# Kernel tuning notes

Hardware: AMD Instinct MI355X
Metric: run time of the kernel (lower is better)

## Reference

```python
import jax, jax.numpy as jnp
import numpy as np

M_RANGE = 2
N_CLASS = 25
IM_CHANNEL = 3


def _conv(x, kernel, pad):
    # torch F.conv2d (cross-correlation), NCHW / OIHW, stride 1, symmetric padding
    return jax.lax.conv_general_dilated(
        x, kernel, window_strides=(1, 1),
        padding=[(pad, pad), (pad, pad)],
        dimension_numbers=('NCHW', 'OIHW', 'NCHW'))


def _label2mask(motion, n_class):
    # motion: [B,1,H,W] int labels -> one-hot mask [B,n_class,H,W]
    oh = jax.nn.one_hot(motion[:, 0], n_class, dtype=jnp.float32)  # [B,H,W,K]
    return jnp.transpose(oh, (0, 3, 1, 2))


def _construct_image(im, m_mask, appear, kernel, pad):
    # im: [B,C,H,W], m_mask: [B,K,H,W], appear: [B,1,H,W]
    im = im * appear
    B, C, H, W = im.shape
    K = m_mask.shape[1]
    # fuse the per-channel / per-sample torch loops into one batched conv
    x = (im[:, :, None] * m_mask[:, None]).reshape(B * C, K, H, W)
    return _conv(x, kernel, pad).reshape(B, C, H, W)


def setup_inputs() -> dict:
    key = jax.random.key(0)
    k1, k2, k3, k4, k5 = jax.random.split(key, 5)
    B, H, W = 32, 192, 192
    return {
        'im_input_f': jax.random.normal(k1, (B, 6, H, W), dtype=jnp.float32),
        'im_input_b': jax.random.normal(k2, (B, 6, H, W), dtype=jnp.float32),
        'gt_motion_f': jax.random.randint(k3, (B, 1, H, W), 0, N_CLASS, dtype=jnp.int64),
        'gt_motion_b': jax.random.randint(k4, (B, 1, H, W), 0, N_CLASS, dtype=jnp.int64),
        'm_kernel': jax.random.uniform(k5, (1, N_CLASS, 2 * M_RANGE + 1, 2 * M_RANGE + 1), dtype=jnp.float32),
    }


def reference(im_input_f, im_input_b, gt_motion_f, gt_motion_b, m_kernel):
    mask_f = _label2mask(gt_motion_f, N_CLASS)
    mask_b = _label2mask(gt_motion_b, N_CLASS)
    seg_f = _conv(mask_f, m_kernel, M_RANGE)  # [B,1,H,W]
    seg_b = _conv(mask_b, m_kernel, M_RANGE)
    appear_f = jax.nn.relu(1.0 - jax.nn.relu(seg_f - 1.0))
    appear_b = jax.nn.relu(1.0 - jax.nn.relu(seg_b - 1.0))
    pred_f = _construct_image(im_input_f[:, -IM_CHANNEL:], mask_f, appear_f, m_kernel, M_RANGE)
    pred_b = _construct_image(im_input_b[:, -IM_CHANNEL:], mask_b, appear_b, m_kernel, M_RANGE)
    seg_f = 1.0 - jax.nn.relu(1.0 - seg_f)
    seg_b = 1.0 - jax.nn.relu(1.0 - seg_b)
    attn = (seg_f + 1e-5) / (seg_f + seg_b + 2e-5)
    pred = attn * pred_f + (1.0 - attn) * pred_b
    return (pred, mask_f, 1.0 - appear_f, attn, mask_b, 1.0 - appear_b, 1.0 - attn)
```

## Files before the change

### kernel.cpp

```cpp
#include <hip/hip_runtime.h>

typedef float f32x4 __attribute__((ext_vector_type(4)));
typedef float f32x2 __attribute__((ext_vector_type(2)));

namespace {
constexpr int BATCH = 32;
constexpr int H = 192;
constexpr int W = 192;
constexpr int HW = H * W;
constexpr int NCLS = 25;
constexpr int LUTN = 26 * 25;

constexpr int OFF_PRED   = 0;
constexpr int OFF_MASKF  = BATCH * 3 * HW;
constexpr int OFF_OMAF   = OFF_MASKF + BATCH * NCLS * HW;
constexpr int OFF_ATTN   = OFF_OMAF + BATCH * HW;
constexpr int OFF_MASKB  = OFF_ATTN + BATCH * HW;
constexpr int OFF_OMAB   = OFF_MASKB + BATCH * NCLS * HW;
constexpr int OFF_OMATTN = OFF_OMAB + BATCH * HW;

constexpr int TY = 8;
constexpr int SROWS = TY + 4;
constexpr int SW = W + 8;
constexpr int GPR = W / 4;
constexpr int NTHR = GPR * TY;
constexpr int YT = H / TY;
constexpr int NBLK = BATCH * YT;
constexpr float SENT = 2.0f * NCLS;
}

__device__ __forceinline__ void nt_store4(float* p, float a, float b, float c, float d) {
    f32x4 v = {a, b, c, d};
    __builtin_nontemporal_store(v, reinterpret_cast<f32x4*>(p));
}

__device__ __forceinline__ void lab_win12(int lw[12], const int* __restrict__ row, int xb) {
    if (xb >= 4) {
        const int4 a = *reinterpret_cast<const int4*>(row + xb - 4);
        lw[0] = a.x; lw[1] = a.y; lw[2] = a.z; lw[3] = a.w;
    } else {
        lw[0] = NCLS; lw[1] = NCLS; lw[2] = NCLS; lw[3] = NCLS;
    }
    {
        const int4 c = *reinterpret_cast<const int4*>(row + xb);
        lw[4] = c.x; lw[5] = c.y; lw[6] = c.z; lw[7] = c.w;
    }
    if (xb <= W - 8) {
        const int4 e = *reinterpret_cast<const int4*>(row + xb + 4);
        lw[8] = e.x; lw[9] = e.y; lw[10] = e.z; lw[11] = e.w;
    } else {
        lw[8] = NCLS; lw[9] = NCLS; lw[10] = NCLS; lw[11] = NCLS;
    }
}

__device__ __forceinline__ void f4_win12(float w[12], const float* __restrict__ row, int xb) {
    if (xb >= 4) {
        const float4 a = *reinterpret_cast<const float4*>(row + xb - 4);
        w[0] = a.x; w[1] = a.y; w[2] = a.z; w[3] = a.w;
    } else {
        w[0] = 0.f; w[1] = 0.f; w[2] = 0.f; w[3] = 0.f;
    }
    {
        const float4 c = *reinterpret_cast<const float4*>(row + xb);
        w[4] = c.x; w[5] = c.y; w[6] = c.z; w[7] = c.w;
    }
    if (xb <= W - 8) {
        const float4 e = *reinterpret_cast<const float4*>(row + xb + 4);
        w[8] = e.x; w[9] = e.y; w[10] = e.z; w[11] = e.w;
    } else {
        w[8] = 0.f; w[9] = 0.f; w[10] = 0.f; w[11] = 0.f;
    }
}

template <bool STORES>
__device__ __forceinline__ void conv_img(
    const float (*P)[SW], const float* __restrict__ im,
    const float* __restrict__ sk, const int lab4[4],
    float* __restrict__ mbase,
    int b, int y, int x, int r_i, int g_i, float acc[3][4])
{
    for (int dy = 0; dy < 5; ++dy) {
        const int yy = y + dy - 2;
        const bool rowok = (yy >= 0 && yy < H);

        float pw[12], v0[12], v1[12], v2[12];
        if (rowok) {
            const int srow = r_i + dy;
            *reinterpret_cast<f32x4*>(&pw[0]) =
                *reinterpret_cast<const f32x4*>(&P[srow][4 * g_i]);
            *reinterpret_cast<f32x4*>(&pw[4]) =
                *reinterpret_cast<const f32x4*>(&P[srow][4 * g_i + 4]);
            *reinterpret_cast<f32x4*>(&pw[8]) =
                *reinterpret_cast<const f32x4*>(&P[srow][4 * g_i + 8]);
            const int imo = b * (6 * HW) + 3 * HW + yy * W;
            f4_win12(v0, im + imo, x);
            f4_win12(v1, im + imo + HW, x);
            f4_win12(v2, im + imo + 2 * HW, x);
        }

        if (STORES) {
#pragma unroll
            for (int kk = 0; kk < 5; ++kk) {
                const int k = dy * 5 + kk;
                nt_store4(mbase + k * HW, lab4[0] == k ? 1.f : 0.f, lab4[1] == k ? 1.f : 0.f,
                          lab4[2] == k ? 1.f : 0.f, lab4[3] == k ? 1.f : 0.f);
            }
        }

        if (rowok) {
            int lw[12];
            float aw[12];
#pragma unroll
            for (int j = 2; j < 10; ++j) {
                const int l = (int)(pw[j] * 0.5f);
                lw[j] = l;
                aw[j] = pw[j] - 2.f * (float)l;
            }
#pragma unroll
            for (int dx = 0; dx < 5; ++dx) {
                const int base = (dy * 5 + dx) * 26;
#pragma unroll
                for (int i = 0; i < 4; ++i) {
                    const int li = i + dx + 2;
                    const float w = aw[li] * sk[base + lw[li]];
                    acc[0][i] = fmaf(w, v0[li], acc[0][i]);
                    acc[1][i] = fmaf(w, v1[li], acc[1][i]);
                    acc[2][i] = fmaf(w, v2[li], acc[2][i]);
                }
            }
        }
    }
}

__global__ __launch_bounds__(NTHR) void k_fused(
    const float* __restrict__ imF, const float* __restrict__ imB,
    const int* __restrict__ labF, const int* __restrict__ labB,
    const float* __restrict__ mk, float* __restrict__ out)
{
    __shared__ float sk[LUTN];
    __shared__ float pF[SROWS][SW];
    __shared__ float pB[SROWS][SW];

    for (int i = threadIdx.x; i < LUTN; i += NTHR) {
        const int tap = i / 26;
        const int l = i - tap * 26;
        sk[i] = (l < NCLS) ? mk[l * 25 + tap] : 0.0f;
    }
    __syncthreads();

    const int blk = blockIdx.x;
    const int by = blk % YT;
    const int b  = blk / YT;
    const int y0 = by * TY;
    const int t = threadIdx.x;
    const int r_i = t / GPR;
    const int g_i = t % GPR;
    const int y = y0 + r_i;
    const int x = 4 * g_i;
    const int pix = b * HW + y * W + x;

    const int4 lfc = *reinterpret_cast<const int4*>(labF + pix);
    const int4 lbc = *reinterpret_cast<const int4*>(labB + pix);
    const int lfa[4] = {lfc.x, lfc.y, lfc.z, lfc.w};
    const int lba[4] = {lbc.x, lbc.y, lbc.z, lbc.w};
    float* __restrict__ mfb = out + OFF_MASKF + b * (NCLS * HW) + y * W + x;

    float segf[4] = {}, segb[4] = {};
#pragma unroll
    for (int dy = 0; dy < 5; ++dy) {
#pragma unroll
        for (int kk = 0; kk < 5; ++kk) {
            const int k = dy * 5 + kk;
            nt_store4(mfb + k * HW, lfa[0] == k ? 1.f : 0.f, lfa[1] == k ? 1.f : 0.f,
                      lfa[2] == k ? 1.f : 0.f, lfa[3] == k ? 1.f : 0.f);
        }
        const int yy = y + dy - 2;
        if (yy >= 0 && yy < H) {
            int lwF[12], lwB[12];
            lab_win12(lwF, labF + b * HW + yy * W, x);
            lab_win12(lwB, labB + b * HW + yy * W, x);
#pragma unroll
            for (int dx = 0; dx < 5; ++dx) {
                const int base = (dy * 5 + dx) * 26;
#pragma unroll
                for (int i = 0; i < 4; ++i) {
                    segf[i] += sk[base + lwF[i + dx + 2]];
                    segb[i] += sk[base + lwB[i + dx + 2]];
                }
            }
        }
    }

    float my_at[4];
    {
        f32x4 pf, pb;
        float af[4], ab[4];
#pragma unroll
        for (int i = 0; i < 4; ++i) {
            af[i] = fmaxf(1.f - fmaxf(segf[i] - 1.f, 0.f), 0.f);
            ab[i] = fmaxf(1.f - fmaxf(segb[i] - 1.f, 0.f), 0.f);
            pf[i] = 2.f * (float)lfa[i] + af[i];
            pb[i] = 2.f * (float)lba[i] + ab[i];
            const float scf = 1.f - fmaxf(1.f - segf[i], 0.f);
            const float scb = 1.f - fmaxf(1.f - segb[i], 0.f);
            my_at[i] = (scf + 1e-5f) / (scf + scb + 2e-5f);
        }
        *reinterpret_cast<f32x4*>(&pF[r_i + 2][4 + x]) = pf;
        *reinterpret_cast<f32x4*>(&pB[r_i + 2][4 + x]) = pb;
        nt_store4(out + OFF_OMAF + pix, 1.f - af[0], 1.f - af[1], 1.f - af[2], 1.f - af[3]);
        nt_store4(out + OFF_OMAB + pix, 1.f - ab[0], 1.f - ab[1], 1.f - ab[2], 1.f - ab[3]);
        nt_store4(out + OFF_ATTN + pix, my_at[0], my_at[1], my_at[2], my_at[3]);
        nt_store4(out + OFF_OMATTN + pix, 1.f - my_at[0], 1.f - my_at[1], 1.f - my_at[2],
                  1.f - my_at[3]);
    }

    {
        const int hrow = t / 96;
        const int row = (hrow < 2) ? hrow : hrow + TY;
        const int hg = t % 96;
        const int xabs = 2 * hg;
        const int xb = xabs & ~3;
        const int off = (hg & 1) * 2;
        const int yabs = y0 + row - 2;
        f32x2 pf2 = {SENT, SENT};
        f32x2 pb2 = {SENT, SENT};
        if (yabs >= 0 && yabs < H) {
            float sf[2] = {0.f, 0.f}, sb[2] = {0.f, 0.f};
            int lf2[2], lb2[2];
            for (int dy = 0; dy < 5; ++dy) {
                const int yy = yabs + dy - 2;
                if (yy < 0 || yy >= H) continue;
                int lwF[12], lwB[12];
                lab_win12(lwF, labF + b * HW + yy * W, xb);
                lab_win12(lwB, labB + b * HW + yy * W, xb);
                if (dy == 2) {
#pragma unroll
                    for (int i = 0; i < 2; ++i) {
                        lf2[i] = lwF[4 + off + i];
                        lb2[i] = lwB[4 + off + i];
                    }
                }
#pragma unroll
                for (int dx = 0; dx < 5; ++dx) {
                    const int base = (dy * 5 + dx) * 26;
#pragma unroll
                    for (int i = 0; i < 2; ++i) {
                        sf[i] += sk[base + lwF[2 + off + i + dx]];
                        sb[i] += sk[base + lwB[2 + off + i + dx]];
                    }
                }
            }
#pragma unroll
            for (int i = 0; i < 2; ++i) {
                const float af = fmaxf(1.f - fmaxf(sf[i] - 1.f, 0.f), 0.f);
                const float ab = fmaxf(1.f - fmaxf(sb[i] - 1.f, 0.f), 0.f);
                pf2[i] = 2.f * (float)lf2[i] + af;
                pb2[i] = 2.f * (float)lb2[i] + ab;
            }
        }
        *reinterpret_cast<f32x2*>(&pF[row][4 + xabs]) = pf2;
        *reinterpret_cast<f32x2*>(&pB[row][4 + xabs]) = pb2;
    }

    if (t < 48) {
        const int arr = t & 1, side = (t >> 1) & 1, row = t >> 2;
        f32x4 s = {SENT, SENT, SENT, SENT};
        float* dst = arr ? &pB[row][side ? W + 4 : 0] : &pF[row][side ? W + 4 : 0];
        *reinterpret_cast<f32x4*>(dst) = s;
    }

    __builtin_amdgcn_sched_barrier(0);
    asm volatile("s_waitcnt lgkmcnt(0)" ::: "memory");
    __builtin_amdgcn_s_barrier();
    __builtin_amdgcn_sched_barrier(0);
    asm volatile("" ::: "memory");

    float accF[3][4] = {};
    float accB[3][4] = {};
    conv_img<false>(pF, imF, sk, lfa, nullptr, b, y, x, r_i, g_i, accF);
    conv_img<true>(pB, imB, sk, lba, out + OFF_MASKB + b * (NCLS * HW) + y * W + x,
                   b, y, x, r_i, g_i, accB);

    float* pout = out + OFF_PRED + b * (3 * HW) + y * W + x;
#pragma unroll
    for (int c = 0; c < 3; ++c) {
        float p[4];
#pragma unroll
        for (int i = 0; i < 4; ++i)
            p[i] = my_at[i] * accF[c][i] + (1.f - my_at[i]) * accB[c][i];
        nt_store4(pout + c * HW, p[0], p[1], p[2], p[3]);
    }
}

extern "C" void kernel_launch(void* const* d_in, const int* in_sizes, int n_in,
                              void* d_out, int out_size, void* d_ws, size_t ws_size,
                              hipStream_t stream) {
    const float* imF  = (const float*)d_in[0];
    const float* imB  = (const float*)d_in[1];
    const int*   labF = (const int*)d_in[2];
    const int*   labB = (const int*)d_in[3];
    const float* mk   = (const float*)d_in[4];
    float* out = (float*)d_out;

    k_fused<<<NBLK, NTHR, 0, stream>>>(imF, imB, labF, labB, mk, out);
}
```

Measured before the change: 71.02 us.

## Stage byte-packed label tiles in shared memory and enlarge row tile

Each block now loads its label rows plus a 4-row halo once into shared memory, packing four labels per 32-bit word. The segmentation conv and the halo recomputation read those packed labels instead of issuing repeated global int4 loads per tap row. The row tile grows from 8 to 12, giving 576 threads per block and fewer blocks, and block indices are swizzled across groups of eight. This adds a shared-memory fill phase and a barrier before compute, and the larger block may lower occupancy.

```diff
diff --git a/kernel.cpp b/kernel.cpp
--- a/kernel.cpp
+++ b/kernel.cpp
@@ -19,38 +19,22 @@
 constexpr int OFF_OMAB   = OFF_MASKB + BATCH * NCLS * HW;
 constexpr int OFF_OMATTN = OFF_OMAB + BATCH * HW;
 
-constexpr int TY = 8;
+constexpr int TY = 12;
 constexpr int SROWS = TY + 4;
 constexpr int SW = W + 8;
 constexpr int GPR = W / 4;
 constexpr int NTHR = GPR * TY;
 constexpr int YT = H / TY;
 constexpr int NBLK = BATCH * YT;
+constexpr int LROWS = TY + 8;
+constexpr int LW32 = 50;
 constexpr float SENT = 2.0f * NCLS;
+constexpr unsigned SENTB = 0x19191919u;
 }
 
 __device__ __forceinline__ void nt_store4(float* p, float a, float b, float c, float d) {
     f32x4 v = {a, b, c, d};
     __builtin_nontemporal_store(v, reinterpret_cast<f32x4*>(p));
-}
-
-__device__ __forceinline__ void lab_win12(int lw[12], const int* __restrict__ row, int xb) {
-    if (xb >= 4) {
-        const int4 a = *reinterpret_cast<const int4*>(row + xb - 4);
-        lw[0] = a.x; lw[1] = a.y; lw[2] = a.z; lw[3] = a.w;
-    } else {
-        lw[0] = NCLS; lw[1] = NCLS; lw[2] = NCLS; lw[3] = NCLS;
-    }
-    {
-        const int4 c = *reinterpret_cast<const int4*>(row + xb);
-        lw[4] = c.x; lw[5] = c.y; lw[6] = c.z; lw[7] = c.w;
-    }
-    if (xb <= W - 8) {
-        const int4 e = *reinterpret_cast<const int4*>(row + xb + 4);
-        lw[8] = e.x; lw[9] = e.y; lw[10] = e.z; lw[11] = e.w;
-    } else {
-        lw[8] = NCLS; lw[9] = NCLS; lw[10] = NCLS; lw[11] = NCLS;
-    }
 }
 
 __device__ __forceinline__ void f4_win12(float w[12], const float* __restrict__ row, int xb) {
@@ -138,31 +122,51 @@
     const float* __restrict__ mk, float* __restrict__ out)
 {
     __shared__ float sk[LUTN];
+    __shared__ unsigned labs[2][LROWS][LW32];
     __shared__ float pF[SROWS][SW];
     __shared__ float pB[SROWS][SW];
 
-    for (int i = threadIdx.x; i < LUTN; i += NTHR) {
-        const int tap = i / 26;
-        const int l = i - tap * 26;
-        sk[i] = (l < NCLS) ? mk[l * 25 + tap] : 0.0f;
-    }
-    __syncthreads();
-
-    const int blk = blockIdx.x;
+    const int o = blockIdx.x;
+    const int blk = (o & 7) * (NBLK / 8) + (o >> 3);
     const int by = blk % YT;
     const int b  = blk / YT;
     const int y0 = by * TY;
     const int t = threadIdx.x;
+
+    for (int i = t; i < LUTN; i += NTHR) {
+        const int tap = i / 26;
+        const int l = i - tap * 26;
+        sk[i] = (l < NCLS) ? mk[l * 25 + tap] : 0.0f;
+    }
+    for (int u = t; u < 2 * LROWS * LW32; u += NTHR) {
+        const int img = u / (LROWS * LW32);
+        const int rem = u - img * (LROWS * LW32);
+        const int row = rem / LW32;
+        const int gw = rem - row * LW32;
+        const int yg = y0 - 4 + row;
+        unsigned v = SENTB;
+        if (yg >= 0 && yg < H && gw > 0 && gw < LW32 - 1) {
+            const int* lp = (img ? labB : labF) + b * HW + yg * W + 4 * (gw - 1);
+            const int4 l4 = *reinterpret_cast<const int4*>(lp);
+            v = (unsigned)(l4.x & 255) | ((unsigned)(l4.y & 255) << 8) |
+                ((unsigned)(l4.z & 255) << 16) | ((unsigned)(l4.w & 255) << 24);
+        }
+        labs[img][row][gw] = v;
+    }
+    __syncthreads();
+
     const int r_i = t / GPR;
     const int g_i = t % GPR;
     const int y = y0 + r_i;
     const int x = 4 * g_i;
     const int pix = b * HW + y * W + x;
 
-    const int4 lfc = *reinterpret_cast<const int4*>(labF + pix);
-    const int4 lbc = *reinterpret_cast<const int4*>(labB + pix);
-    const int lfa[4] = {lfc.x, lfc.y, lfc.z, lfc.w};
-    const int lba[4] = {lbc.x, lbc.y, lbc.z, lbc.w};
+    const unsigned cf = labs[0][r_i + 4][g_i + 1];
+    const unsigned cb = labs[1][r_i + 4][g_i + 1];
+    const int lfa[4] = {(int)(cf & 255), (int)((cf >> 8) & 255),
+                        (int)((cf >> 16) & 255), (int)((cf >> 24) & 255)};
+    const int lba[4] = {(int)(cb & 255), (int)((cb >> 8) & 255),
+                        (int)((cb >> 16) & 255), (int)((cb >> 24) & 255)};
     float* __restrict__ mfb = out + OFF_MASKF + b * (NCLS * HW) + y * W + x;
 
     float segf[4] = {}, segb[4] = {};
@@ -174,19 +178,28 @@
             nt_store4(mfb + k * HW, lfa[0] == k ? 1.f : 0.f, lfa[1] == k ? 1.f : 0.f,
                       lfa[2] == k ? 1.f : 0.f, lfa[3] == k ? 1.f : 0.f);
         }
-        const int yy = y + dy - 2;
-        if (yy >= 0 && yy < H) {
-            int lwF[12], lwB[12];
-            lab_win12(lwF, labF + b * HW + yy * W, x);
-            lab_win12(lwB, labB + b * HW + yy * W, x);
-#pragma unroll
-            for (int dx = 0; dx < 5; ++dx) {
-                const int base = (dy * 5 + dx) * 26;
-#pragma unroll
-                for (int i = 0; i < 4; ++i) {
-                    segf[i] += sk[base + lwF[i + dx + 2]];
-                    segb[i] += sk[base + lwB[i + dx + 2]];
-                }
+        const int sr = r_i + dy + 2;
+        const unsigned f0 = labs[0][sr][g_i], f1 = labs[0][sr][g_i + 1],
+                       f2 = labs[0][sr][g_i + 2];
+        const unsigned h0 = labs[1][sr][g_i], h1 = labs[1][sr][g_i + 1],
+                       h2 = labs[1][sr][g_i + 2];
+        int lwF[8], lwB[8];
+#pragma unroll
+        for (int j = 0; j < 8; ++j) {
+            const int bo = 2 + j;
+            const unsigned wf = (bo < 4) ? f0 : (bo < 8 ? f1 : f2);
+            const unsigned wb = (bo < 4) ? h0 : (bo < 8 ? h1 : h2);
+            const int sh = (bo & 3) * 8;
+            lwF[j] = (int)((wf >> sh) & 255);
+            lwB[j] = (int)((wb >> sh) & 255);
+        }
+#pragma unroll
+        for (int dx = 0; dx < 5; ++dx) {
+            const int base = (dy * 5 + dx) * 26;
+#pragma unroll
+            for (int i = 0; i < 4; ++i) {
+                segf[i] += sk[base + lwF[i + dx]];
+                segb[i] += sk[base + lwB[i + dx]];
             }
         }
     }
@@ -214,55 +227,58 @@
                   1.f - my_at[3]);
     }
 
-    {
+    if (t < 384) {
         const int hrow = t / 96;
         const int row = (hrow < 2) ? hrow : hrow + TY;
         const int hg = t % 96;
-        const int xabs = 2 * hg;
-        const int xb = xabs & ~3;
-        const int off = (hg & 1) * 2;
-        const int yabs = y0 + row - 2;
-        f32x2 pf2 = {SENT, SENT};
-        f32x2 pb2 = {SENT, SENT};
-        if (yabs >= 0 && yabs < H) {
-            float sf[2] = {0.f, 0.f}, sb[2] = {0.f, 0.f};
-            int lf2[2], lb2[2];
-            for (int dy = 0; dy < 5; ++dy) {
-                const int yy = yabs + dy - 2;
-                if (yy < 0 || yy >= H) continue;
-                int lwF[12], lwB[12];
-                lab_win12(lwF, labF + b * HW + yy * W, xb);
-                lab_win12(lwB, labB + b * HW + yy * W, xb);
-                if (dy == 2) {
-#pragma unroll
-                    for (int i = 0; i < 2; ++i) {
-                        lf2[i] = lwF[4 + off + i];
-                        lb2[i] = lwB[4 + off + i];
-                    }
-                }
-#pragma unroll
-                for (int dx = 0; dx < 5; ++dx) {
-                    const int base = (dy * 5 + dx) * 26;
-#pragma unroll
-                    for (int i = 0; i < 2; ++i) {
-                        sf[i] += sk[base + lwF[2 + off + i + dx]];
-                        sb[i] += sk[base + lwB[2 + off + i + dx]];
-                    }
-                }
-            }
-#pragma unroll
-            for (int i = 0; i < 2; ++i) {
-                const float af = fmaxf(1.f - fmaxf(sf[i] - 1.f, 0.f), 0.f);
-                const float ab = fmaxf(1.f - fmaxf(sb[i] - 1.f, 0.f), 0.f);
-                pf2[i] = 2.f * (float)lf2[i] + af;
-                pb2[i] = 2.f * (float)lb2[i] + ab;
-            }
-        }
-        *reinterpret_cast<f32x2*>(&pF[row][4 + xabs]) = pf2;
-        *reinterpret_cast<f32x2*>(&pB[row][4 + xabs]) = pb2;
-    }
-
-    if (t < 48) {
+        const int xs = 2 * hg;
+        const int q = xs >> 2;
+        const int off0 = (xs & 3) + 2;
+        float sf[2] = {0.f, 0.f}, sb[2] = {0.f, 0.f};
+#pragma unroll
+        for (int dyh = 0; dyh < 5; ++dyh) {
+            const int sr = row + dyh;
+            const unsigned f0 = labs[0][sr][q], f1 = labs[0][sr][q + 1],
+                           f2 = labs[0][sr][q + 2];
+            const unsigned h0 = labs[1][sr][q], h1 = labs[1][sr][q + 1],
+                           h2 = labs[1][sr][q + 2];
+            int lf6[6], lb6[6];
+#pragma unroll
+            for (int j = 0; j < 6; ++j) {
+                const int bo = off0 + j;
+                const unsigned wf = (bo < 4) ? f0 : (bo < 8 ? f1 : f2);
+                const unsigned wb = (bo < 4) ? h0 : (bo < 8 ? h1 : h2);
+                const int sh = (bo & 3) * 8;
+                lf6[j] = (int)((wf >> sh) & 255);
+                lb6[j] = (int)((wb >> sh) & 255);
+            }
+#pragma unroll
+            for (int dx = 0; dx < 5; ++dx) {
+                const int base = (dyh * 5 + dx) * 26;
+                sf[0] += sk[base + lf6[dx]];
+                sf[1] += sk[base + lf6[dx + 1]];
+                sb[0] += sk[base + lb6[dx]];
+                sb[1] += sk[base + lb6[dx + 1]];
+            }
+        }
+        const unsigned cf2 = labs[0][row + 2][q + 1];
+        const unsigned cb2 = labs[1][row + 2][q + 1];
+        const int shc = (xs & 3) * 8;
+        const int lf2[2] = {(int)((cf2 >> shc) & 255), (int)((cf2 >> (shc + 8)) & 255)};
+        const int lb2[2] = {(int)((cb2 >> shc) & 255), (int)((cb2 >> (shc + 8)) & 255)};
+        f32x2 pf2, pb2;
+#pragma unroll
+        for (int i = 0; i < 2; ++i) {
+            const float af = fmaxf(1.f - fmaxf(sf[i] - 1.f, 0.f), 0.f);
+            const float ab = fmaxf(1.f - fmaxf(sb[i] - 1.f, 0.f), 0.f);
+            pf2[i] = 2.f * (float)lf2[i] + af;
+            pb2[i] = 2.f * (float)lb2[i] + ab;
+        }
+        *reinterpret_cast<f32x2*>(&pF[row][4 + xs]) = pf2;
+        *reinterpret_cast<f32x2*>(&pB[row][4 + xs]) = pb2;
+    }
+
+    if (t < 64) {
         const int arr = t & 1, side = (t >> 1) & 1, row = t >> 2;
         f32x4 s = {SENT, SENT, SENT, SENT};
         float* dst = arr ? &pB[row][side ? W + 4 : 0] : &pF[row][side ? W + 4 : 0];
```

Result: faster. 61.14 us (median of 2 runs) (-13.9%).
